# Optimization experiments

Hardware: AMD Instinct MI355X
Metric: run time of the kernel (lower is better)

Reference implementation:

```python
import jax, jax.numpy as jnp
import numpy as np

N = 30000      # input points
M = 7500       # sampled queries = floor(N * ratio), ratio=0.25
K = 16         # neighbors per query
D_X = 64       # input feature dim
D_REL = 64     # point_pos_nn output dim
D_F = D_X + D_REL  # fij_hat dim = 128


def setup_inputs() -> dict:
    key = jax.random.key(0)
    ks = jax.random.split(key, 6)
    x = jax.random.normal(ks[0], (N, D_X), jnp.float32)
    pos = jax.random.normal(ks[1], (N, 3), jnp.float32)
    idx = jax.random.randint(ks[2], (M,), 0, N)
    W_pos = jax.random.normal(ks[3], (10, D_REL), jnp.float32) / jnp.sqrt(10.0)
    b_pos = jnp.zeros((D_REL,), jnp.float32)
    W_att = jax.random.normal(ks[4], (D_F, D_F), jnp.float32) / jnp.sqrt(float(D_F))
    b_att = jnp.zeros((D_F,), jnp.float32)
    W_glob = jax.random.normal(ks[5], (D_F, D_F), jnp.float32) / jnp.sqrt(float(D_F))
    b_glob = jnp.zeros((D_F,), jnp.float32)
    return {"x": x, "pos": pos, "idx": idx, "W_pos": W_pos, "b_pos": b_pos,
            "W_att": W_att, "b_att": b_att, "W_glob": W_glob, "b_glob": b_glob}


def reference(x, pos, idx, W_pos, b_pos, W_att, b_att, W_glob, b_glob):
    # --- KNN: brute-force squared distances from sampled queries to all points ---
    pos_q = pos[idx]                                         # [M, 3]
    d2 = ((pos_q * pos_q).sum(-1)[:, None]
          + (pos * pos).sum(-1)[None, :]
          - 2.0 * pos_q @ pos.T)                             # [M, N]
    _, nbr = jax.lax.top_k(-d2, K)                           # [M, K] neighbor indices

    # --- Local Spatial Encoding (message) ---
    pos_j = pos[nbr]                                         # [M, K, 3]
    pos_i = jnp.broadcast_to(pos_q[:, None, :], pos_j.shape) # [M, K, 3]
    vij = pos_i - pos_j                                      # [M, K, 3]
    dij = jnp.linalg.norm(vij, axis=-1, keepdims=True)       # [M, K, 1]
    rel = jnp.concatenate([pos_i, pos_j, vij, dij], axis=-1) # [M, K, 10]
    rij = jax.nn.relu(rel @ W_pos + b_pos)                   # [M, K, D_REL]

    # --- Attentive pooling ---
    fij = jnp.concatenate([x[nbr], rij], axis=-1)            # [M, K, D_F]
    g = fij @ W_att + b_att                                  # [M, K, D_F]
    s = jax.nn.softmax(g, axis=-1)                           # softmax over feature dim
    aggr = jnp.mean(s * fij, axis=1)                         # mean over K neighbors -> [M, D_F]

    # --- global_nn (update) ---
    return jax.nn.relu(aggr @ W_glob + b_glob)               # [M, D_F]
```

## Files before the change

### kernel.cpp

```cpp
#include <hip/hip_runtime.h>
#include <stdint.h>

#define KQ    8
#define CAP   512
#define KNN_T 256
#define KNB   16

typedef short short8 __attribute__((ext_vector_type(8)));
typedef float floatx4 __attribute__((ext_vector_type(4)));
typedef float floatx2 __attribute__((ext_vector_type(2)));

__device__ __forceinline__ unsigned short f2bf(float x) {
  union { float f; uint32_t u; } v; v.f = x;
  uint32_t u = v.u + 0x7FFFu + ((v.u >> 16) & 1u);
  return (unsigned short)(u >> 16);
}
__device__ __forceinline__ float bf2f(unsigned short b) {
  return __uint_as_float(((uint32_t)b) << 16);
}

static __device__ __forceinline__ floatx2 fma2(floatx2 a, floatx2 b, floatx2 c) {
#if __has_builtin(__builtin_elementwise_fma)
  return __builtin_elementwise_fma(a, b, c);
#else
  floatx2 r; r[0] = fmaf(a[0], b[0], c[0]); r[1] = fmaf(a[1], b[1], c[1]);
  return r;
#endif
}
static __device__ __forceinline__ floatx2 min2(floatx2 a, floatx2 b) {
#if __has_builtin(__builtin_elementwise_min)
  return __builtin_elementwise_min(a, b);
#else
  floatx2 r; r[0] = fminf(a[0], b[0]); r[1] = fminf(a[1], b[1]);
  return r;
#endif
}
static __device__ __forceinline__ floatx2 sp2(float v) {
  floatx2 r; r[0] = v; r[1] = v; return r;
}

__global__ void prep_kernel(const float* __restrict__ x,
                            const float* __restrict__ pos,
                            const float* __restrict__ W_att,
                            unsigned short* __restrict__ xb,
                            float4* __restrict__ pos4,
                            float* __restrict__ pospk,
                            unsigned short* __restrict__ Wt, int N, int Npad2) {
  int id = blockIdx.x * 256 + threadIdx.x;
  int nx8 = N * 8;
  if (id < nx8) {
    const float4* src = (const float4*)x + (size_t)id * 2;
    float4 a = src[0], b = src[1];
    short8 v;
    v[0] = (short)f2bf(a.x); v[1] = (short)f2bf(a.y);
    v[2] = (short)f2bf(a.z); v[3] = (short)f2bf(a.w);
    v[4] = (short)f2bf(b.x); v[5] = (short)f2bf(b.y);
    v[6] = (short)f2bf(b.z); v[7] = (short)f2bf(b.w);
    *(short8*)(xb + (size_t)id * 8) = v;
  } else if (id < nx8 + Npad2) {
    int j = id - nx8;
    float px = 0.f, py = 0.f, pz = 0.f, pp = 3.0e38f;
    if (j < N) {
      px = pos[3 * j]; py = pos[3 * j + 1]; pz = pos[3 * j + 2];
      pp = fmaf(px, px, fmaf(py, py, pz * pz));
      pos4[j] = make_float4(px, py, pz, pp);
    }
    int pair = j >> 1, h = j & 1;
    float* dst = pospk + (size_t)pair * 8;
    dst[0 + h] = px; dst[2 + h] = py; dst[4 + h] = pz; dst[6 + h] = pp;
  } else if (id < nx8 + Npad2 + 128 * 128) {
    int t = id - nx8 - Npad2;
    int c = t >> 7, f = t & 127;
    Wt[f * 128 + c] = f2bf(W_att[t]);
  }
}

__global__ __launch_bounds__(KNN_T) void knn_kernel(
    const float4* __restrict__ pos4, const float4* __restrict__ pospk4,
    const int* __restrict__ idx, int* __restrict__ nbr, int Npad2, int M) {
  __shared__ uint32_t cand[KQ][CAP];
  __shared__ int cnt[KQ];
  __shared__ float gmin[KQ][16];
  __shared__ float tau_s[KQ];
  __shared__ float4 qpos_s[KQ];

  const int tid = threadIdx.x;
  const int q0  = blockIdx.x * KQ;
  const int iters = Npad2 >> 9;

  float sx[KQ], sy[KQ], sz[KQ];
#pragma unroll
  for (int qi = 0; qi < KQ; ++qi) {
    int m = q0 + qi; if (m >= M) m = M - 1;
    float4 qp = pos4[idx[m]];
    sx[qi] = -2.f * qp.x; sy[qi] = -2.f * qp.y; sz[qi] = -2.f * qp.z;
    if (tid == qi) qpos_s[qi] = qp;
  }
  if (tid < KQ) cnt[tid] = 0;

  floatx2 tmn[KQ];
#pragma unroll
  for (int qi = 0; qi < KQ; ++qi) tmn[qi] = sp2(3.4e38f);
  {
    float4 a = pospk4[tid * 2], b = pospk4[tid * 2 + 1];
    for (int it = 0; it < iters; ++it) {
      float4 an = a, bn = b;
      if (it + 1 < iters) {
        int nb = (it + 1) * 512 + tid * 2;
        an = pospk4[nb]; bn = pospk4[nb + 1];
      }
      floatx2 X, Y, Z, W;
      X[0] = a.x; X[1] = a.y; Y[0] = a.z; Y[1] = a.w;
      Z[0] = b.x; Z[1] = b.y; W[0] = b.z; W[1] = b.w;
#pragma unroll
      for (int qi = 0; qi < KQ; ++qi) {
        floatx2 t = fma2(sp2(sx[qi]), X,
                         fma2(sp2(sy[qi]), Y, fma2(sp2(sz[qi]), Z, W)));
        tmn[qi] = min2(tmn[qi], t);
      }
      a = an; b = bn;
    }
  }
#pragma unroll
  for (int qi = 0; qi < KQ; ++qi) {
    float v = fminf(tmn[qi][0], tmn[qi][1]);
    v = fminf(v, __shfl_xor(v, 1));
    v = fminf(v, __shfl_xor(v, 2));
    v = fminf(v, __shfl_xor(v, 4));
    v = fminf(v, __shfl_xor(v, 8));
    if ((tid & 15) == 0) gmin[qi][tid >> 4] = v;
  }
  __syncthreads();
  if (tid < KQ) {
    float t = gmin[tid][0];
#pragma unroll
    for (int g = 1; g < 16; ++g) t = fmaxf(t, gmin[tid][g]);
    tau_s[tid] = t + fabsf(t) * 1e-6f + 1e-7f;
  }
  __syncthreads();
  float tau[KQ];
#pragma unroll
  for (int qi = 0; qi < KQ; ++qi) tau[qi] = tau_s[qi];

  {
    float4 a = pospk4[tid * 2], b = pospk4[tid * 2 + 1];
    for (int it = 0; it < iters; ++it) {
      float4 an = a, bn = b;
      if (it + 1 < iters) {
        int nb = (it + 1) * 512 + tid * 2;
        an = pospk4[nb]; bn = pospk4[nb + 1];
      }
      floatx2 X, Y, Z, W;
      X[0] = a.x; X[1] = a.y; Y[0] = a.z; Y[1] = a.w;
      Z[0] = b.x; Z[1] = b.y; W[0] = b.z; W[1] = b.w;
      const int j0 = (it * 256 + tid) * 2;
#pragma unroll
      for (int qi = 0; qi < KQ; ++qi) {
        floatx2 t = fma2(sp2(sx[qi]), X,
                         fma2(sp2(sy[qi]), Y, fma2(sp2(sz[qi]), Z, W)));
        if (fminf(t[0], t[1]) <= tau[qi]) {
          if (t[0] <= tau[qi]) {
            int sl = atomicAdd(&cnt[qi], 1);
            if (sl < CAP) cand[qi][sl] = (uint32_t)j0;
          }
          if (t[1] <= tau[qi]) {
            int sl = atomicAdd(&cnt[qi], 1);
            if (sl < CAP) cand[qi][sl] = (uint32_t)(j0 + 1);
          }
        }
      }
      a = an; b = bn;
    }
  }
  __syncthreads();

  const int wv = tid >> 6, ln = tid & 63;
#pragma unroll
  for (int i = 0; i < 2; ++i) {
    int ql = wv * 2 + i;
    int mq = q0 + ql;
    int nc = cnt[ql]; if (nc > CAP) nc = CAP;
    float4 qp = qpos_s[ql];
    unsigned long long c[CAP / 64];
#pragma unroll
    for (int ch = 0; ch < CAP / 64; ++ch) c[ch] = ~0ull;
#pragma unroll
    for (int ch = 0; ch < CAP / 64; ++ch) {
      int s = ch * 64 + ln;
      if (s < nc) {
        uint32_t j = cand[ql][s];
        float4 pj = pos4[j];
        float dot = fmaf(qp.x, pj.x, fmaf(qp.y, pj.y, qp.z * pj.z));
        float tt  = fmaf(-2.f, dot, pj.w);
        float d2  = fmaxf(qp.w + tt, 0.f);
        c[ch] = ((unsigned long long)__float_as_uint(d2) << 32) | j;
      }
    }
#pragma unroll
    for (int r = 0; r < KNB; ++r) {
      unsigned long long mn = c[0];
#pragma unroll
      for (int ch = 1; ch < CAP / 64; ++ch) mn = (c[ch] < mn) ? c[ch] : mn;
#pragma unroll
      for (int off = 1; off < 64; off <<= 1) {
        unsigned long long o = __shfl_xor(mn, off);
        mn = (o < mn) ? o : mn;
      }
      if (mq < M && ln == 0) nbr[mq * KNB + r] = (int)(uint32_t)mn;
#pragma unroll
      for (int ch = 0; ch < CAP / 64; ++ch)
        if (c[ch] == mn) c[ch] = ~0ull;
    }
  }
}

__global__ __launch_bounds__(256) void mid_kernel(
    const unsigned short* __restrict__ xb, const float4* __restrict__ pos4,
    const int* __restrict__ idx, const float* __restrict__ W_pos,
    const float* __restrict__ b_pos, const unsigned short* __restrict__ Wt,
    const float* __restrict__ b_att, const int* __restrict__ nbr,
    float* __restrict__ aggr, int M) {
  __shared__ __align__(16) unsigned short fijb[8][16][136];
  __shared__ int nbr_s[128];
  __shared__ float4 qpos_s[8];

  const int tid = threadIdx.x;
  const int wid = tid >> 6, lane = tid & 63;
  const int col = lane & 15, quad = lane >> 4;
  const int b = blockIdx.x;

  if (tid < 128) {
    int mq = b * 8 + (tid >> 4); if (mq >= M) mq = M - 1;
    nbr_s[tid] = nbr[mq * 16 + (tid & 15)];
  }
  if (tid < 8) {
    int mq = b * 8 + tid; if (mq >= M) mq = M - 1;
    qpos_s[tid] = pos4[idx[mq]];
  }
  float wp[10];
#pragma unroll
  for (int t = 0; t < 10; ++t) wp[t] = W_pos[t * 64 + lane];
  float bp = b_pos[lane];
  __syncthreads();

  {
    int rr = tid >> 1, h = tid & 1;
    int jn = nbr_s[rr];
    const short8* src = (const short8*)(xb + ((size_t)jn << 6) + (h << 5));
    short8 v0 = src[0], v1 = src[1], v2 = src[2], v3 = src[3];
    short8* dst = (short8*)&fijb[rr >> 4][rr & 15][h * 32];
    dst[0] = v0; dst[1] = v1; dst[2] = v2; dst[3] = v3;
  }
#pragma unroll
  for (int qi = 0; qi < 2; ++qi) {
    int q = wid * 2 + qi;
    float4 qp = qpos_s[q];
#pragma unroll 4
    for (int k = 0; k < 16; ++k) {
      int jn = nbr_s[q * 16 + k];
      float4 pj = pos4[jn];
      float vx = qp.x - pj.x, vy = qp.y - pj.y, vz = qp.z - pj.z;
      float dd = sqrtf(fmaf(vx, vx, fmaf(vy, vy, vz * vz)));
      float r = bp;
      r = fmaf(qp.x, wp[0], r); r = fmaf(qp.y, wp[1], r); r = fmaf(qp.z, wp[2], r);
      r = fmaf(pj.x, wp[3], r); r = fmaf(pj.y, wp[4], r); r = fmaf(pj.z, wp[5], r);
      r = fmaf(vx, wp[6], r);  r = fmaf(vy, wp[7], r);  r = fmaf(vz, wp[8], r);
      r = fmaf(dd, wp[9], r);
      r = fmaxf(r, 0.f);
      fijb[q][k][64 + lane] = f2bf(r);
    }
  }
  __syncthreads();

#pragma unroll 1
  for (int qi = 0; qi < 2; ++qi) {
    int q = wid * 2 + qi;
    int mq = b * 8 + q;

    short8 af[4];
#pragma unroll
    for (int cs = 0; cs < 4; ++cs)
      af[cs] = *(const short8*)&fijb[q][col][cs * 32 + quad * 8];

    floatx4 acc[8];
#pragma unroll
    for (int ft = 0; ft < 8; ++ft) {
      float bav = b_att[ft * 16 + col];
      floatx4 a = {bav, bav, bav, bav};
#pragma unroll
      for (int cs = 0; cs < 4; ++cs) {
        short8 bfrag =
            *(const short8*)&Wt[(ft * 16 + col) * 128 + cs * 32 + quad * 8];
        a = __builtin_amdgcn_mfma_f32_16x16x32_bf16(af[cs], bfrag, a, 0, 0, 0);
      }
      acc[ft] = a;
    }

    float rowmax[4], rowinv[4];
#pragma unroll
    for (int r = 0; r < 4; ++r) {
      float mx = acc[0][r];
#pragma unroll
      for (int ft = 1; ft < 8; ++ft) mx = fmaxf(mx, acc[ft][r]);
      mx = fmaxf(mx, __shfl_xor(mx, 1));
      mx = fmaxf(mx, __shfl_xor(mx, 2));
      mx = fmaxf(mx, __shfl_xor(mx, 4));
      mx = fmaxf(mx, __shfl_xor(mx, 8));
      float sm = 0.f;
#pragma unroll
      for (int ft = 0; ft < 8; ++ft) sm += __expf(acc[ft][r] - mx);
      sm += __shfl_xor(sm, 1);
      sm += __shfl_xor(sm, 2);
      sm += __shfl_xor(sm, 4);
      sm += __shfl_xor(sm, 8);
      rowmax[r] = mx;
      rowinv[r] = 1.0f / sm;
    }

#pragma unroll
    for (int ft = 0; ft < 8; ++ft) {
      float ap = 0.f;
#pragma unroll
      for (int r = 0; r < 4; ++r) {
        float s = __expf(acc[ft][r] - rowmax[r]) * rowinv[r];
        float fv = bf2f(fijb[q][quad * 4 + r][ft * 16 + col]);
        ap = fmaf(s, fv, ap);
      }
      ap += __shfl_xor(ap, 16);
      ap += __shfl_xor(ap, 32);
      if (quad == 0 && mq < M)
        aggr[mq * 128 + ft * 16 + col] = ap * (1.0f / 16.0f);
    }
  }
}

__global__ __launch_bounds__(256) void out_kernel(
    const float* __restrict__ aggr, const float* __restrict__ W_glob,
    const float* __restrict__ b_glob, float* __restrict__ out, int M) {
  __shared__ float ag[16][128];
  const int tid = threadIdx.x;
  const int mbase = blockIdx.x * 16;
  for (int s = tid; s < 16 * 128; s += 256) {
    int r = s >> 7, cc = s & 127;
    int m = mbase + r;
    ((float*)ag)[s] = (m < M) ? aggr[m * 128 + cc] : 0.0f;
  }
  __syncthreads();
  const int f = tid & 127, h = tid >> 7;
  float acc[8];
  float bg = b_glob[f];
#pragma unroll
  for (int i = 0; i < 8; ++i) acc[i] = bg;
  for (int c = 0; c < 128; c += 4) {
    float w0 = W_glob[(c + 0) * 128 + f];
    float w1 = W_glob[(c + 1) * 128 + f];
    float w2 = W_glob[(c + 2) * 128 + f];
    float w3 = W_glob[(c + 3) * 128 + f];
#pragma unroll
    for (int i = 0; i < 8; ++i) {
      const floatx4 a4 = *(const floatx4*)&ag[h * 8 + i][c];
      acc[i] += a4[0] * w0 + a4[1] * w1 + a4[2] * w2 + a4[3] * w3;
    }
  }
#pragma unroll
  for (int i = 0; i < 8; ++i) {
    int m = mbase + h * 8 + i;
    if (m < M) out[m * 128 + f] = fmaxf(acc[i], 0.0f);
  }
}

extern "C" void kernel_launch(void* const* d_in, const int* in_sizes, int n_in,
                              void* d_out, int out_size, void* d_ws,
                              size_t ws_size, hipStream_t stream) {
  const float* x      = (const float*)d_in[0];
  const float* pos    = (const float*)d_in[1];
  const int*   idx    = (const int*)d_in[2];
  const float* W_pos  = (const float*)d_in[3];
  const float* b_pos  = (const float*)d_in[4];
  const float* W_att  = (const float*)d_in[5];
  const float* b_att  = (const float*)d_in[6];
  const float* W_glob = (const float*)d_in[7];
  const float* b_glob = (const float*)d_in[8];
  float* out = (float*)d_out;

  const int N = in_sizes[1] / 3;
  const int M = in_sizes[2];
  const int Npad2 = (N + 511) & ~511;

  char* ws = (char*)d_ws;
  size_t o = 0;
  float4* pos4 = (float4*)(ws + o);               o += ((size_t)N * 16 + 255) & ~(size_t)255;
  unsigned short* xb = (unsigned short*)(ws + o); o += ((size_t)N * 128 + 255) & ~(size_t)255;
  float* pospk = (float*)(ws + o);                o += ((size_t)Npad2 * 16 + 255) & ~(size_t)255;
  unsigned short* Wt = (unsigned short*)(ws + o); o += (128 * 128 * 2 + 255) & ~(size_t)255;
  int* nbr = (int*)(ws + o);                      o += (((size_t)M * KNB * 4) + 255) & ~(size_t)255;
  float* aggr = (float*)(ws + o);

  int prep_ids = N * 8 + Npad2 + 128 * 128;
  prep_kernel<<<(prep_ids + 255) / 256, 256, 0, stream>>>(
      x, pos, W_att, xb, pos4, pospk, Wt, N, Npad2);
  knn_kernel<<<(M + KQ - 1) / KQ, KNN_T, 0, stream>>>(
      pos4, (const float4*)pospk, idx, nbr, Npad2, M);
  mid_kernel<<<(M + 7) / 8, 256, 0, stream>>>(xb, pos4, idx, W_pos, b_pos, Wt,
                                              b_att, nbr, aggr, M);
  out_kernel<<<(M + 15) / 16, 256, 0, stream>>>(aggr, W_glob, b_glob, out, M);
}
```

Before: 229.1 us.

## Split KNN scan across point chunks with global candidate merge kernel

```diff
diff --git a/kernel.cpp b/kernel.cpp
--- a/kernel.cpp
+++ b/kernel.cpp
@@ -1,10 +1,11 @@
 #include <hip/hip_runtime.h>
 #include <stdint.h>
 
-#define KQ    8
-#define CAP   512
-#define KNN_T 256
-#define KNB   16
+#define KQ     8
+#define KNB    16
+#define CAPC   256
+#define CAPG   512
+#define NCHUNK 4
 
 typedef short short8 __attribute__((ext_vector_type(8)));
 typedef float floatx4 __attribute__((ext_vector_type(4)));
@@ -17,6 +18,9 @@
 }
 __device__ __forceinline__ float bf2f(unsigned short b) {
   return __uint_as_float(((uint32_t)b) << 16);
+}
+__device__ __forceinline__ float rfl(float v) {
+  return __int_as_float(__builtin_amdgcn_readfirstlane(__float_as_int(v)));
 }
 
 static __device__ __forceinline__ floatx2 fma2(floatx2 a, floatx2 b, floatx2 c) {
@@ -39,26 +43,15 @@
   floatx2 r; r[0] = v; r[1] = v; return r;
 }
 
-__global__ void prep_kernel(const float* __restrict__ x,
-                            const float* __restrict__ pos,
+__global__ void prep_kernel(const float* __restrict__ pos,
                             const float* __restrict__ W_att,
-                            unsigned short* __restrict__ xb,
                             float4* __restrict__ pos4,
                             float* __restrict__ pospk,
-                            unsigned short* __restrict__ Wt, int N, int Npad2) {
+                            unsigned short* __restrict__ Wt,
+                            int* __restrict__ cnt_g, int N, int Npad2, int M) {
   int id = blockIdx.x * 256 + threadIdx.x;
-  int nx8 = N * 8;
-  if (id < nx8) {
-    const float4* src = (const float4*)x + (size_t)id * 2;
-    float4 a = src[0], b = src[1];
-    short8 v;
-    v[0] = (short)f2bf(a.x); v[1] = (short)f2bf(a.y);
-    v[2] = (short)f2bf(a.z); v[3] = (short)f2bf(a.w);
-    v[4] = (short)f2bf(b.x); v[5] = (short)f2bf(b.y);
-    v[6] = (short)f2bf(b.z); v[7] = (short)f2bf(b.w);
-    *(short8*)(xb + (size_t)id * 8) = v;
-  } else if (id < nx8 + Npad2) {
-    int j = id - nx8;
+  if (id < Npad2) {
+    int j = id;
     float px = 0.f, py = 0.f, pz = 0.f, pp = 3.0e38f;
     if (j < N) {
       px = pos[3 * j]; py = pos[3 * j + 1]; pz = pos[3 * j + 2];
@@ -68,33 +61,39 @@
     int pair = j >> 1, h = j & 1;
     float* dst = pospk + (size_t)pair * 8;
     dst[0 + h] = px; dst[2 + h] = py; dst[4 + h] = pz; dst[6 + h] = pp;
-  } else if (id < nx8 + Npad2 + 128 * 128) {
-    int t = id - nx8 - Npad2;
+  } else if (id < Npad2 + 128 * 128) {
+    int t = id - Npad2;
     int c = t >> 7, f = t & 127;
     Wt[f * 128 + c] = f2bf(W_att[t]);
-  }
-}
-
-__global__ __launch_bounds__(KNN_T) void knn_kernel(
+  } else if (id < Npad2 + 128 * 128 + M) {
+    cnt_g[id - Npad2 - 128 * 128] = 0;
+  }
+}
+
+__global__ __launch_bounds__(256) void knn_kernel(
     const float4* __restrict__ pos4, const float4* __restrict__ pospk4,
-    const int* __restrict__ idx, int* __restrict__ nbr, int Npad2, int M) {
-  __shared__ uint32_t cand[KQ][CAP];
+    const int* __restrict__ idx, uint32_t* __restrict__ cand_g,
+    int* __restrict__ cnt_g, int Npad2, int M) {
+  __shared__ uint32_t cand[KQ][CAPC];
   __shared__ int cnt[KQ];
   __shared__ float gmin[KQ][16];
   __shared__ float tau_s[KQ];
-  __shared__ float4 qpos_s[KQ];
 
   const int tid = threadIdx.x;
-  const int q0  = blockIdx.x * KQ;
-  const int iters = Npad2 >> 9;
+  const int wid = tid >> 6, lane = tid & 63;
+  const int qg = blockIdx.x >> 2, chunk = blockIdx.x & 3;
+  const int q0 = qg * KQ;
+  const int iters = Npad2 >> 11;
+  const int pbase = chunk * (Npad2 >> 3);
+  const int jbase = chunk * (Npad2 >> 2);
 
   float sx[KQ], sy[KQ], sz[KQ];
 #pragma unroll
   for (int qi = 0; qi < KQ; ++qi) {
     int m = q0 + qi; if (m >= M) m = M - 1;
     float4 qp = pos4[idx[m]];
-    sx[qi] = -2.f * qp.x; sy[qi] = -2.f * qp.y; sz[qi] = -2.f * qp.z;
-    if (tid == qi) qpos_s[qi] = qp;
+    sx[qi] = rfl(-2.f * qp.x); sy[qi] = rfl(-2.f * qp.y);
+    sz[qi] = rfl(-2.f * qp.z);
   }
   if (tid < KQ) cnt[tid] = 0;
 
@@ -102,12 +101,13 @@
 #pragma unroll
   for (int qi = 0; qi < KQ; ++qi) tmn[qi] = sp2(3.4e38f);
   {
-    float4 a = pospk4[tid * 2], b = pospk4[tid * 2 + 1];
+    int pg = (pbase + tid) * 2;
+    float4 a = pospk4[pg], b = pospk4[pg + 1];
     for (int it = 0; it < iters; ++it) {
       float4 an = a, bn = b;
       if (it + 1 < iters) {
-        int nb = (it + 1) * 512 + tid * 2;
-        an = pospk4[nb]; bn = pospk4[nb + 1];
+        int pgn = (pbase + (it + 1) * 256 + tid) * 2;
+        an = pospk4[pgn]; bn = pospk4[pgn + 1];
       }
       floatx2 X, Y, Z, W;
       X[0] = a.x; X[1] = a.y; Y[0] = a.z; Y[1] = a.w;
@@ -140,20 +140,21 @@
   __syncthreads();
   float tau[KQ];
 #pragma unroll
-  for (int qi = 0; qi < KQ; ++qi) tau[qi] = tau_s[qi];
+  for (int qi = 0; qi < KQ; ++qi) tau[qi] = rfl(tau_s[qi]);
 
   {
-    float4 a = pospk4[tid * 2], b = pospk4[tid * 2 + 1];
+    int pg = (pbase + tid) * 2;
+    float4 a = pospk4[pg], b = pospk4[pg + 1];
     for (int it = 0; it < iters; ++it) {
       float4 an = a, bn = b;
       if (it + 1 < iters) {
-        int nb = (it + 1) * 512 + tid * 2;
-        an = pospk4[nb]; bn = pospk4[nb + 1];
+        int pgn = (pbase + (it + 1) * 256 + tid) * 2;
+        an = pospk4[pgn]; bn = pospk4[pgn + 1];
       }
       floatx2 X, Y, Z, W;
       X[0] = a.x; X[1] = a.y; Y[0] = a.z; Y[1] = a.w;
       Z[0] = b.x; Z[1] = b.y; W[0] = b.z; W[1] = b.w;
-      const int j0 = (it * 256 + tid) * 2;
+      const int j0 = jbase + it * 512 + tid * 2;
 #pragma unroll
       for (int qi = 0; qi < KQ; ++qi) {
         floatx2 t = fma2(sp2(sx[qi]), X,
@@ -161,11 +162,11 @@
         if (fminf(t[0], t[1]) <= tau[qi]) {
           if (t[0] <= tau[qi]) {
             int sl = atomicAdd(&cnt[qi], 1);
-            if (sl < CAP) cand[qi][sl] = (uint32_t)j0;
+            if (sl < CAPC) cand[qi][sl] = (uint32_t)j0;
           }
           if (t[1] <= tau[qi]) {
             int sl = atomicAdd(&cnt[qi], 1);
-            if (sl < CAP) cand[qi][sl] = (uint32_t)(j0 + 1);
+            if (sl < CAPC) cand[qi][sl] = (uint32_t)(j0 + 1);
           }
         }
       }
@@ -174,48 +175,68 @@
   }
   __syncthreads();
 
-  const int wv = tid >> 6, ln = tid & 63;
 #pragma unroll
   for (int i = 0; i < 2; ++i) {
-    int ql = wv * 2 + i;
-    int mq = q0 + ql;
-    int nc = cnt[ql]; if (nc > CAP) nc = CAP;
-    float4 qp = qpos_s[ql];
-    unsigned long long c[CAP / 64];
-#pragma unroll
-    for (int ch = 0; ch < CAP / 64; ++ch) c[ch] = ~0ull;
-#pragma unroll
-    for (int ch = 0; ch < CAP / 64; ++ch) {
-      int s = ch * 64 + ln;
-      if (s < nc) {
-        uint32_t j = cand[ql][s];
-        float4 pj = pos4[j];
-        float dot = fmaf(qp.x, pj.x, fmaf(qp.y, pj.y, qp.z * pj.z));
-        float tt  = fmaf(-2.f, dot, pj.w);
-        float d2  = fmaxf(qp.w + tt, 0.f);
-        c[ch] = ((unsigned long long)__float_as_uint(d2) << 32) | j;
-      }
-    }
-#pragma unroll
-    for (int r = 0; r < KNB; ++r) {
-      unsigned long long mn = c[0];
-#pragma unroll
-      for (int ch = 1; ch < CAP / 64; ++ch) mn = (c[ch] < mn) ? c[ch] : mn;
-#pragma unroll
-      for (int off = 1; off < 64; off <<= 1) {
-        unsigned long long o = __shfl_xor(mn, off);
-        mn = (o < mn) ? o : mn;
-      }
-      if (mq < M && ln == 0) nbr[mq * KNB + r] = (int)(uint32_t)mn;
-#pragma unroll
-      for (int ch = 0; ch < CAP / 64; ++ch)
-        if (c[ch] == mn) c[ch] = ~0ull;
-    }
+    int qi = wid * 2 + i;
+    int m = q0 + qi;
+    if (m < M) {
+      int nc = cnt[qi]; if (nc > CAPC) nc = CAPC;
+      int base = 0;
+      if (lane == 0) base = atomicAdd(&cnt_g[m], nc);
+      base = __shfl(base, 0);
+      for (int s = lane; s < nc; s += 64) {
+        int p = base + s;
+        if (p < CAPG) cand_g[(size_t)m * CAPG + p] = cand[qi][s];
+      }
+    }
+  }
+}
+
+__global__ __launch_bounds__(256) void merge_kernel(
+    const float4* __restrict__ pos4, const int* __restrict__ idx,
+    const uint32_t* __restrict__ cand_g, const int* __restrict__ cnt_g,
+    int* __restrict__ nbr, int M) {
+  const int tid = threadIdx.x;
+  const int lane = tid & 63;
+  const int m = blockIdx.x * 4 + (tid >> 6);
+  if (m >= M) return;
+
+  float4 qp = pos4[idx[m]];
+  int nc = cnt_g[m]; if (nc > CAPG) nc = CAPG;
+
+  unsigned long long c[CAPG / 64];
+#pragma unroll
+  for (int ch = 0; ch < CAPG / 64; ++ch) {
+    c[ch] = ~0ull;
+    int s = ch * 64 + lane;
+    if (s < nc) {
+      uint32_t j = cand_g[(size_t)m * CAPG + s];
+      float4 pj = pos4[j];
+      float dot = fmaf(qp.x, pj.x, fmaf(qp.y, pj.y, qp.z * pj.z));
+      float tt  = fmaf(-2.f, dot, pj.w);
+      float d2  = fmaxf(qp.w + tt, 0.f);
+      c[ch] = ((unsigned long long)__float_as_uint(d2) << 32) | j;
+    }
+  }
+#pragma unroll
+  for (int r = 0; r < KNB; ++r) {
+    unsigned long long mn = c[0];
+#pragma unroll
+    for (int ch = 1; ch < CAPG / 64; ++ch) mn = (c[ch] < mn) ? c[ch] : mn;
+#pragma unroll
+    for (int off = 1; off < 64; off <<= 1) {
+      unsigned long long o = __shfl_xor(mn, off);
+      mn = (o < mn) ? o : mn;
+    }
+    if (lane == 0) nbr[m * KNB + r] = (int)(uint32_t)mn;
+#pragma unroll
+    for (int ch = 0; ch < CAPG / 64; ++ch)
+      if (c[ch] == mn) c[ch] = ~0ull;
   }
 }
 
 __global__ __launch_bounds__(256) void mid_kernel(
-    const unsigned short* __restrict__ xb, const float4* __restrict__ pos4,
+    const float* __restrict__ x, const float4* __restrict__ pos4,
     const int* __restrict__ idx, const float* __restrict__ W_pos,
     const float* __restrict__ b_pos, const unsigned short* __restrict__ Wt,
     const float* __restrict__ b_att, const int* __restrict__ nbr,
@@ -246,10 +267,18 @@
   {
     int rr = tid >> 1, h = tid & 1;
     int jn = nbr_s[rr];
-    const short8* src = (const short8*)(xb + ((size_t)jn << 6) + (h << 5));
-    short8 v0 = src[0], v1 = src[1], v2 = src[2], v3 = src[3];
+    const float4* src = (const float4*)(x + (size_t)jn * 64) + h * 8;
     short8* dst = (short8*)&fijb[rr >> 4][rr & 15][h * 32];
-    dst[0] = v0; dst[1] = v1; dst[2] = v2; dst[3] = v3;
+#pragma unroll
+    for (int i = 0; i < 4; ++i) {
+      float4 u = src[2 * i], v = src[2 * i + 1];
+      short8 w;
+      w[0] = (short)f2bf(u.x); w[1] = (short)f2bf(u.y);
+      w[2] = (short)f2bf(u.z); w[3] = (short)f2bf(u.w);
+      w[4] = (short)f2bf(v.x); w[5] = (short)f2bf(v.y);
+      w[6] = (short)f2bf(v.z); w[7] = (short)f2bf(v.w);
+      dst[i] = w;
+    }
   }
 #pragma unroll
   for (int qi = 0; qi < 2; ++qi) {
@@ -385,23 +414,26 @@
 
   const int N = in_sizes[1] / 3;
   const int M = in_sizes[2];
-  const int Npad2 = (N + 511) & ~511;
+  const int Npad2 = (N + 2047) & ~2047;
 
   char* ws = (char*)d_ws;
   size_t o = 0;
   float4* pos4 = (float4*)(ws + o);               o += ((size_t)N * 16 + 255) & ~(size_t)255;
-  unsigned short* xb = (unsigned short*)(ws + o); o += ((size_t)N * 128 + 255) & ~(size_t)255;
   float* pospk = (float*)(ws + o);                o += ((size_t)Npad2 * 16 + 255) & ~(size_t)255;
   unsigned short* Wt = (unsigned short*)(ws + o); o += (128 * 128 * 2 + 255) & ~(size_t)255;
   int* nbr = (int*)(ws + o);                      o += (((size_t)M * KNB * 4) + 255) & ~(size_t)255;
+  uint32_t* cand_g = (uint32_t*)(ws + o);         o += (((size_t)M * CAPG * 4) + 255) & ~(size_t)255;
+  int* cnt_g = (int*)(ws + o);                    o += (((size_t)M * 4) + 255) & ~(size_t)255;
   float* aggr = (float*)(ws + o);
 
-  int prep_ids = N * 8 + Npad2 + 128 * 128;
+  int prep_ids = Npad2 + 128 * 128 + M;
   prep_kernel<<<(prep_ids + 255) / 256, 256, 0, stream>>>(
-      x, pos, W_att, xb, pos4, pospk, Wt, N, Npad2);
-  knn_kernel<<<(M + KQ - 1) / KQ, KNN_T, 0, stream>>>(
-      pos4, (const float4*)pospk, idx, nbr, Npad2, M);
-  mid_kernel<<<(M + 7) / 8, 256, 0, stream>>>(xb, pos4, idx, W_pos, b_pos, Wt,
+      pos, W_att, pos4, pospk, Wt, cnt_g, N, Npad2, M);
+  knn_kernel<<<((M + KQ - 1) / KQ) * NCHUNK, 256, 0, stream>>>(
+      pos4, (const float4*)pospk, idx, cand_g, cnt_g, Npad2, M);
+  merge_kernel<<<(M + 3) / 4, 256, 0, stream>>>(pos4, idx, cand_g, cnt_g, nbr,
+                                                M);
+  mid_kernel<<<(M + 7) / 8, 256, 0, stream>>>(x, pos4, idx, W_pos, b_pos, Wt,
                                               b_att, nbr, aggr, M);
   out_kernel<<<(M + 15) / 16, 256, 0, stream>>>(aggr, W_glob, b_glob, out, M);
 }
```

Measured after the change: 242.5 us. +5.8%, slower.
